# Performance work log

Hardware: AMD Instinct MI355X
Metric: run time of the kernel (lower is better)

The kernel has to match this reference:

```python
import jax, jax.numpy as jnp
import numpy as np

EPS = 1e-5
N, F, D = 16384, 1024, 8


def setup_inputs() -> dict:
    key = jax.random.key(0)
    k1, k2, k3, k4 = jax.random.split(key, 4)
    x = jax.random.normal(k1, (N, F), dtype=jnp.float32)
    y = jax.random.randint(k2, (N,), 0, D, dtype=jnp.int64)
    # per-domain affine params (BatchNorm1d weight/bias per domain)
    gamma = 1.0 + 0.1 * jax.random.normal(k3, (D, F), dtype=jnp.float32)
    beta = 0.1 * jax.random.normal(k4, (D, F), dtype=jnp.float32)
    return {"x": x, "y": y, "gamma": gamma, "beta": beta}


def reference(x, y, gamma, beta):
    # Domain-specific batchnorm (training mode): per-domain batch stats,
    # biased variance, affine. Domains with 1 sample pass through x;
    # domains with 0 samples contribute nothing (out stays zero).
    d = gamma.shape[0]
    ones = jnp.ones((x.shape[0],), dtype=x.dtype)
    counts = jax.ops.segment_sum(ones, y, num_segments=d)          # [D]
    s1 = jax.ops.segment_sum(x, y, num_segments=d)                 # [D, F]
    s2 = jax.ops.segment_sum(x * x, y, num_segments=d)             # [D, F]
    cnt = jnp.maximum(counts, 1.0)[:, None]                        # avoid /0
    mean = s1 / cnt                                                # [D, F]
    var = s2 / cnt - mean * mean                                   # biased var
    inv = jax.lax.rsqrt(var + EPS)                                 # [D, F]
    xhat = (x - mean[y]) * inv[y]                                  # [N, F]
    out_bn = gamma[y] * xhat + beta[y]
    c = counts[y][:, None]                                         # [N, 1]
    return jnp.where(c > 1.0, out_bn, jnp.where(c == 1.0, x, jnp.zeros_like(x)))
```

## Files before the change

### kernel.cpp

```cpp
#include <hip/hip_runtime.h>


#define EPSV 1e-5f
constexpr int N = 16384;
constexpr int F = 1024;
constexpr int D = 8;
constexpr int ROWS_PER_BLOCK = 64;
constexpr int RG = N / ROWS_PER_BLOCK;

__global__ __launch_bounds__(256) void k1_partials(
    const float* __restrict__ x, const int* __restrict__ y,
    float* __restrict__ partials, int* __restrict__ cnt_parts) {
  const int t = threadIdx.x;
  const int rg = blockIdx.x >> 1;
  const int h = blockIdx.x & 1;

  __shared__ int hist[D];
  if (t < D) hist[t] = 0;
  __syncthreads();
  if (h == 0 && t < ROWS_PER_BLOCK) {
    int d = y[rg * ROWS_PER_BLOCK + t];
    atomicAdd(&hist[d], 1);
  }
  __syncthreads();
  if (h == 0 && t < D) cnt_parts[rg * D + t] = hist[t];

  float2 a1[D], a2[D];
#pragma unroll
  for (int k = 0; k < D; ++k) {
    a1[k] = make_float2(0.f, 0.f);
    a2[k] = make_float2(0.f, 0.f);
  }

  const float2* __restrict__ x2 = (const float2*)x;
  const int col2 = h * 256 + t;
  const int row0 = rg * ROWS_PER_BLOCK;

#define ACC(K)                            \
  a1[K].x += v.x;                         \
  a1[K].y += v.y;                         \
  a2[K].x = fmaf(v.x, v.x, a2[K].x);      \
  a2[K].y = fmaf(v.y, v.y, a2[K].y);      \
  break;

  for (int r = 0; r < ROWS_PER_BLOCK; r += 8) {
    const int n = row0 + r;
    int dd[8];
    float2 vv[8];
#pragma unroll
    for (int j = 0; j < 8; ++j) dd[j] = y[n + j];
#pragma unroll
    for (int j = 0; j < 8; ++j) vv[j] = x2[(n + j) * 512 + col2];
#pragma unroll
    for (int j = 0; j < 8; ++j) {
      float2 v = vv[j];
      switch (dd[j]) {
        case 0: ACC(0)
        case 1: ACC(1)
        case 2: ACC(2)
        case 3: ACC(3)
        case 4: ACC(4)
        case 5: ACC(5)
        case 6: ACC(6)
        case 7: ACC(7)
      }
    }
  }
#undef ACC

  float4* __restrict__ p4 = (float4*)partials;
#pragma unroll
  for (int k = 0; k < D; ++k) {
    float4 w = make_float4(a1[k].x, a2[k].x, a1[k].y, a2[k].y);
    p4[(rg * D + k) * 512 + h * 256 + t] = w;
  }
}

__global__ __launch_bounds__(256) void k2_stats(
    const float* __restrict__ partials, const int* __restrict__ cnt_parts,
    const float* __restrict__ gamma, const float* __restrict__ beta,
    float* __restrict__ scale, float* __restrict__ shift) {
  const int t = threadIdx.x;
  const int i = t & 31;
  const int ch = t >> 5;
  const int p = blockIdx.x * 32 + i;
  const int d = p >> 10;

  __shared__ int sc[256];
  sc[t] = cnt_parts[t * D + d];

  const float2* __restrict__ pp = (const float2*)partials;
  float s1 = 0.f, s2 = 0.f;
#pragma unroll 8
  for (int r = 0; r < 32; ++r) {
    const int rg = ch * 32 + r;
    float2 v = pp[(size_t)rg * (D * F) + p];
    s1 += v.x;
    s2 += v.y;
  }

  __shared__ float sf[8][32][2];
  sf[ch][i][0] = s1;
  sf[ch][i][1] = s2;
  __syncthreads();
  for (int s = 128; s > 0; s >>= 1) {
    if (t < s) sc[t] += sc[t + s];
    __syncthreads();
  }

  if (t < 32) {
    float r1 = 0.f, r2 = 0.f;
#pragma unroll
    for (int c = 0; c < 8; ++c) {
      r1 += sf[c][t][0];
      r2 += sf[c][t][1];
    }
    const int pw = blockIdx.x * 32 + t;
    const float c = (float)sc[0];
    const float cc = fmaxf(c, 1.f);
    const float mean = r1 / cc;
    const float var = r2 / cc - mean * mean;
    const float inv = rsqrtf(var + EPSV);
    float scv = gamma[pw] * inv;
    float shv = beta[pw] - mean * scv;
    if (c <= 1.f) {
      scv = (c == 1.f) ? 1.f : 0.f;
      shv = 0.f;
    }
    scale[pw] = scv;
    shift[pw] = shv;
  }
}

__global__ __launch_bounds__(256) void k3_apply(
    const float* __restrict__ x, const int* __restrict__ y,
    const float* __restrict__ scale, const float* __restrict__ shift,
    float* __restrict__ out) {
  const int t = threadIdx.x;
  const int n0 = blockIdx.x * 8;

  int dd[8];
#pragma unroll
  for (int j = 0; j < 8; ++j) dd[j] = y[n0 + j];

#pragma unroll
  for (int j = 0; j < 8; ++j) {
    const int n = n0 + j;
    const float4 v = ((const float4*)x)[n * 256 + t];
    const float4 g = ((const float4*)scale)[dd[j] * 256 + t];
    const float4 b = ((const float4*)shift)[dd[j] * 256 + t];
    float4 o;
    o.x = fmaf(v.x, g.x, b.x);
    o.y = fmaf(v.y, g.y, b.y);
    o.z = fmaf(v.z, g.z, b.z);
    o.w = fmaf(v.w, g.w, b.w);
    ((float4*)out)[n * 256 + t] = o;
  }
}

extern "C" void kernel_launch(void* const* d_in, const int* in_sizes, int n_in,
                              void* d_out, int out_size, void* d_ws, size_t ws_size,
                              hipStream_t stream) {
  const float* x = (const float*)d_in[0];
  const int* y = (const int*)d_in[1];
  const float* gamma = (const float*)d_in[2];
  const float* beta = (const float*)d_in[3];
  float* out = (float*)d_out;

  float* partials = (float*)d_ws;
  int* cnt_parts = (int*)(partials + (size_t)RG * D * F * 2);
  float* scale = (float*)(cnt_parts + RG * D);
  float* shift = scale + D * F;

  k1_partials<<<RG * 2, 256, 0, stream>>>(x, y, partials, cnt_parts);
  k2_stats<<<256, 256, 0, stream>>>(partials, cnt_parts, gamma, beta, scale, shift);
  k3_apply<<<N / 8, 256, 0, stream>>>(x, y, scale, shift, out);
}
```

Measured before the change: 136.1 us.

## Fuse three BN kernels into one cooperative kernel with grid syncs

Merges the partial-sum, stats and apply kernels into one cooperative kernel of 256 blocks, separated by two grid-wide syncs. Rows per block in the partial phase double to 128, which halves the partial buffer the stats phase reads. The apply phase now has each block handle 64 rows instead of 8. The aim is to remove two kernel launch gaps and reduce partial traffic, at the cost of grid-sync overhead and only 256 resident blocks during the bandwidth-bound apply phase.

```diff
diff --git a/kernel.cpp b/kernel.cpp
--- a/kernel.cpp
+++ b/kernel.cpp
@@ -1,40 +1,51 @@
 #include <hip/hip_runtime.h>
+#include <hip/hip_cooperative_groups.h>
+
+namespace cg = cooperative_groups;
 
 
 #define EPSV 1e-5f
 constexpr int N = 16384;
 constexpr int F = 1024;
 constexpr int D = 8;
-constexpr int ROWS_PER_BLOCK = 64;
-constexpr int RG = N / ROWS_PER_BLOCK;
+constexpr int RPB = 128;
+constexpr int RG = N / RPB;
+constexpr int GRID = RG * 2;
 
-__global__ __launch_bounds__(256) void k1_partials(
+__global__ __launch_bounds__(256) void ds_bn_fused(
     const float* __restrict__ x, const int* __restrict__ y,
-    float* __restrict__ partials, int* __restrict__ cnt_parts) {
+    const float* __restrict__ gamma, const float* __restrict__ beta,
+    float* __restrict__ out, float* __restrict__ partials,
+    int* __restrict__ cnt_parts, float* __restrict__ scale,
+    float* __restrict__ shift) {
+  cg::grid_group gg = cg::this_grid();
   const int t = threadIdx.x;
-  const int rg = blockIdx.x >> 1;
-  const int h = blockIdx.x & 1;
+  const int b = blockIdx.x;
 
   __shared__ int hist[D];
-  if (t < D) hist[t] = 0;
-  __syncthreads();
-  if (h == 0 && t < ROWS_PER_BLOCK) {
-    int d = y[rg * ROWS_PER_BLOCK + t];
-    atomicAdd(&hist[d], 1);
-  }
-  __syncthreads();
-  if (h == 0 && t < D) cnt_parts[rg * D + t] = hist[t];
+  __shared__ int sc[256];
+  __shared__ float sf[8][32][2];
 
-  float2 a1[D], a2[D];
+  {
+    const int rg = b >> 1;
+    const int h = b & 1;
+
+    if (t < D) hist[t] = 0;
+    __syncthreads();
+    if (h == 0 && t < RPB) atomicAdd(&hist[y[rg * RPB + t]], 1);
+    __syncthreads();
+    if (h == 0 && t < D) cnt_parts[rg * D + t] = hist[t];
+
+    float2 a1[D], a2[D];
 #pragma unroll
-  for (int k = 0; k < D; ++k) {
-    a1[k] = make_float2(0.f, 0.f);
-    a2[k] = make_float2(0.f, 0.f);
-  }
+    for (int k = 0; k < D; ++k) {
+      a1[k] = make_float2(0.f, 0.f);
+      a2[k] = make_float2(0.f, 0.f);
+    }
 
-  const float2* __restrict__ x2 = (const float2*)x;
-  const int col2 = h * 256 + t;
-  const int row0 = rg * ROWS_PER_BLOCK;
+    const float2* __restrict__ x2 = (const float2*)x;
+    const int col2 = h * 256 + t;
+    const int row0 = rg * RPB;
 
 #define ACC(K)                            \
   a1[K].x += v.x;                         \
@@ -43,118 +54,113 @@
   a2[K].y = fmaf(v.y, v.y, a2[K].y);      \
   break;
 
-  for (int r = 0; r < ROWS_PER_BLOCK; r += 8) {
-    const int n = row0 + r;
-    int dd[8];
-    float2 vv[8];
+    for (int r = 0; r < RPB; r += 8) {
+      const int n = row0 + r;
+      int dd[8];
+      float2 vv[8];
 #pragma unroll
-    for (int j = 0; j < 8; ++j) dd[j] = y[n + j];
+      for (int j = 0; j < 8; ++j) dd[j] = y[n + j];
 #pragma unroll
-    for (int j = 0; j < 8; ++j) vv[j] = x2[(n + j) * 512 + col2];
+      for (int j = 0; j < 8; ++j) vv[j] = x2[(size_t)(n + j) * 512 + col2];
 #pragma unroll
-    for (int j = 0; j < 8; ++j) {
-      float2 v = vv[j];
-      switch (dd[j]) {
-        case 0: ACC(0)
-        case 1: ACC(1)
-        case 2: ACC(2)
-        case 3: ACC(3)
-        case 4: ACC(4)
-        case 5: ACC(5)
-        case 6: ACC(6)
-        case 7: ACC(7)
+      for (int j = 0; j < 8; ++j) {
+        float2 v = vv[j];
+        switch (dd[j]) {
+          case 0: ACC(0)
+          case 1: ACC(1)
+          case 2: ACC(2)
+          case 3: ACC(3)
+          case 4: ACC(4)
+          case 5: ACC(5)
+          case 6: ACC(6)
+          case 7: ACC(7)
+        }
       }
     }
-  }
 #undef ACC
 
-  float4* __restrict__ p4 = (float4*)partials;
+    float4* __restrict__ p4 = (float4*)partials;
 #pragma unroll
-  for (int k = 0; k < D; ++k) {
-    float4 w = make_float4(a1[k].x, a2[k].x, a1[k].y, a2[k].y);
-    p4[(rg * D + k) * 512 + h * 256 + t] = w;
-  }
-}
-
-__global__ __launch_bounds__(256) void k2_stats(
-    const float* __restrict__ partials, const int* __restrict__ cnt_parts,
-    const float* __restrict__ gamma, const float* __restrict__ beta,
-    float* __restrict__ scale, float* __restrict__ shift) {
-  const int t = threadIdx.x;
-  const int i = t & 31;
-  const int ch = t >> 5;
-  const int p = blockIdx.x * 32 + i;
-  const int d = p >> 10;
-
-  __shared__ int sc[256];
-  sc[t] = cnt_parts[t * D + d];
-
-  const float2* __restrict__ pp = (const float2*)partials;
-  float s1 = 0.f, s2 = 0.f;
-#pragma unroll 8
-  for (int r = 0; r < 32; ++r) {
-    const int rg = ch * 32 + r;
-    float2 v = pp[(size_t)rg * (D * F) + p];
-    s1 += v.x;
-    s2 += v.y;
+    for (int k = 0; k < D; ++k) {
+      float4 w = make_float4(a1[k].x, a2[k].x, a1[k].y, a2[k].y);
+      p4[(rg * D + k) * 512 + h * 256 + t] = w;
+    }
   }
 
-  __shared__ float sf[8][32][2];
-  sf[ch][i][0] = s1;
-  sf[ch][i][1] = s2;
-  __syncthreads();
-  for (int s = 128; s > 0; s >>= 1) {
-    if (t < s) sc[t] += sc[t + s];
+  gg.sync();
+
+  {
+    const int i = t & 31;
+    const int ch = t >> 5;
+    const int p = b * 32 + i;
+    const int d = p >> 10;
+
+    sc[t] = (t < RG) ? cnt_parts[t * D + d] : 0;
+
+    const float2* __restrict__ pp = (const float2*)partials;
+    float s1 = 0.f, s2 = 0.f;
+#pragma unroll
+    for (int r = 0; r < 16; ++r) {
+      const int rg = ch * 16 + r;
+      float2 v = pp[(size_t)rg * (D * F) + p];
+      s1 += v.x;
+      s2 += v.y;
+    }
+
+    sf[ch][i][0] = s1;
+    sf[ch][i][1] = s2;
     __syncthreads();
+    for (int s = 128; s > 0; s >>= 1) {
+      if (t < s) sc[t] += sc[t + s];
+      __syncthreads();
+    }
+
+    if (t < 32) {
+      float r1 = 0.f, r2 = 0.f;
+#pragma unroll
+      for (int c = 0; c < 8; ++c) {
+        r1 += sf[c][t][0];
+        r2 += sf[c][t][1];
+      }
+      const int pw = b * 32 + t;
+      const float c = (float)sc[0];
+      const float cc = fmaxf(c, 1.f);
+      const float mean = r1 / cc;
+      const float var = r2 / cc - mean * mean;
+      const float inv = rsqrtf(var + EPSV);
+      float scv = gamma[pw] * inv;
+      float shv = beta[pw] - mean * scv;
+      if (c <= 1.f) {
+        scv = (c == 1.f) ? 1.f : 0.f;
+        shv = 0.f;
+      }
+      scale[pw] = scv;
+      shift[pw] = shv;
+    }
   }
 
-  if (t < 32) {
-    float r1 = 0.f, r2 = 0.f;
+  gg.sync();
+
+  {
+    const int n0 = b * 64;
+    for (int r = 0; r < 64; r += 8) {
+      int dd[8];
 #pragma unroll
-    for (int c = 0; c < 8; ++c) {
-      r1 += sf[c][t][0];
-      r2 += sf[c][t][1];
+      for (int j = 0; j < 8; ++j) dd[j] = y[n0 + r + j];
+#pragma unroll
+      for (int j = 0; j < 8; ++j) {
+        const int n = n0 + r + j;
+        const float4 v = ((const float4*)x)[(size_t)n * 256 + t];
+        const float4 g = ((const float4*)scale)[dd[j] * 256 + t];
+        const float4 bb = ((const float4*)shift)[dd[j] * 256 + t];
+        float4 o;
+        o.x = fmaf(v.x, g.x, bb.x);
+        o.y = fmaf(v.y, g.y, bb.y);
+        o.z = fmaf(v.z, g.z, bb.z);
+        o.w = fmaf(v.w, g.w, bb.w);
+        ((float4*)out)[(size_t)n * 256 + t] = o;
+      }
     }
-    const int pw = blockIdx.x * 32 + t;
-    const float c = (float)sc[0];
-    const float cc = fmaxf(c, 1.f);
-    const float mean = r1 / cc;
-    const float var = r2 / cc - mean * mean;
-    const float inv = rsqrtf(var + EPSV);
-    float scv = gamma[pw] * inv;
-    float shv = beta[pw] - mean * scv;
-    if (c <= 1.f) {
-      scv = (c == 1.f) ? 1.f : 0.f;
-      shv = 0.f;
-    }
-    scale[pw] = scv;
-    shift[pw] = shv;
-  }
-}
-
-__global__ __launch_bounds__(256) void k3_apply(
-    const float* __restrict__ x, const int* __restrict__ y,
-    const float* __restrict__ scale, const float* __restrict__ shift,
-    float* __restrict__ out) {
-  const int t = threadIdx.x;
-  const int n0 = blockIdx.x * 8;
-
-  int dd[8];
-#pragma unroll
-  for (int j = 0; j < 8; ++j) dd[j] = y[n0 + j];
-
-#pragma unroll
-  for (int j = 0; j < 8; ++j) {
-    const int n = n0 + j;
-    const float4 v = ((const float4*)x)[n * 256 + t];
-    const float4 g = ((const float4*)scale)[dd[j] * 256 + t];
-    const float4 b = ((const float4*)shift)[dd[j] * 256 + t];
-    float4 o;
-    o.x = fmaf(v.x, g.x, b.x);
-    o.y = fmaf(v.y, g.y, b.y);
-    o.z = fmaf(v.z, g.z, b.z);
-    o.w = fmaf(v.w, g.w, b.w);
-    ((float4*)out)[n * 256 + t] = o;
   }
 }
 
@@ -172,7 +178,9 @@
   float* scale = (float*)(cnt_parts + RG * D);
   float* shift = scale + D * F;
 
-  k1_partials<<<RG * 2, 256, 0, stream>>>(x, y, partials, cnt_parts);
-  k2_stats<<<256, 256, 0, stream>>>(partials, cnt_parts, gamma, beta, scale, shift);
-  k3_apply<<<N / 8, 256, 0, stream>>>(x, y, scale, shift, out);
+  void* args[] = {(void*)&x,   (void*)&y,         (void*)&gamma,
+                  (void*)&beta, (void*)&out,      (void*)&partials,
+                  (void*)&cnt_parts, (void*)&scale, (void*)&shift};
+  hipLaunchCooperativeKernel((const void*)ds_bn_fused, dim3(GRID), dim3(256),
+                             args, 0, stream);
 }
```

Measured after the change: 218.9 us. +60.8%, slower.
